# Kernel optimization log

Hardware: AMD Instinct MI355X
Metric: run time of the kernel (lower is better)

The kernel has to match this reference:

```python
import jax, jax.numpy as jnp
import numpy as np

N = 50000      # nodes
E = 800000     # edges (before self-loops)
F_IN = 256     # num_features
H = 8          # heads (conv1)
C = 32         # hidden_size per head (conv1)
OUT = 2        # conv2 out channels (1 head)
NEG_SLOPE = 0.2


def setup_inputs() -> dict:
    key = jax.random.key(0)
    ks = jax.random.split(key, 12)
    x = jax.random.normal(ks[0], (N, F_IN), jnp.float32)
    edge_index = jax.random.randint(ks[1], (2, E), 0, N, dtype=jnp.int64)

    def glorot(k, shape):
        fan = shape[0] if len(shape) == 2 else int(np.prod(shape))
        s = float(np.sqrt(6.0 / (fan + shape[-1])))
        return jax.random.uniform(k, shape, jnp.float32, -s, s)

    W1 = glorot(ks[2], (F_IN, H * C))
    att_src1 = glorot(ks[3], (H, C))
    att_dst1 = glorot(ks[4], (H, C))
    b1 = jnp.zeros((H * C,), jnp.float32)
    W2 = glorot(ks[5], (H * C, 1 * OUT))
    att_src2 = glorot(ks[6], (1, OUT))
    att_dst2 = glorot(ks[7], (1, OUT))
    b2 = jnp.zeros((OUT,), jnp.float32)
    return {"x": x, "edge_index": edge_index, "W1": W1, "att_src1": att_src1,
            "att_dst1": att_dst1, "b1": b1, "W2": W2, "att_src2": att_src2,
            "att_dst2": att_dst2, "b2": b2}


def gat_conv(x, src, dst, W, a_src, a_dst, b, heads, ch, n):
    # x: [n, f] -> projected [n, heads, ch]
    xp = (x @ W).reshape(n, heads, ch)
    alpha_src = jnp.einsum('nhc,hc->nh', xp, a_src)   # [n, H]
    alpha_dst = jnp.einsum('nhc,hc->nh', xp, a_dst)   # [n, H]
    e = jax.nn.leaky_relu(alpha_src[src] + alpha_dst[dst], NEG_SLOPE)  # [E', H]
    # segment softmax over edges grouped by destination node
    m = jax.ops.segment_max(e, dst, num_segments=n)                    # [n, H]
    p = jnp.exp(e - m[dst])
    denom = jax.ops.segment_sum(p, dst, num_segments=n)                # [n, H]
    alpha = p / denom[dst]                                             # [E', H]
    # weighted scatter-aggregate of source messages
    out = jax.ops.segment_sum(xp[src] * alpha[:, :, None], dst, num_segments=n)
    return out.reshape(n, heads * ch) + b


def reference(x, edge_index, W1, att_src1, att_dst1, b1, W2, att_src2, att_dst2, b2):
    n = x.shape[0]
    loops = jnp.arange(n, dtype=edge_index.dtype)  # GATConv add_self_loops=True
    src = jnp.concatenate([edge_index[0], loops])
    dst = jnp.concatenate([edge_index[1], loops])
    h = jax.nn.relu(gat_conv(x, src, dst, W1, att_src1, att_dst1, b1, H, C, n))
    # eval mode: F.dropout and attention dropout are identity
    return gat_conv(h, src, dst, W2, att_src2, att_dst2, b2, 1, OUT, n)
```

## Files before the change

kernel.cpp:

```cpp
#include <hip/hip_runtime.h>
#include <math.h>

#define N_NODES 50000
#define N_EDGES 800000
#define EP (N_EDGES + N_NODES)
#define NEG 0.2f
#define SCAN_BLOCKS 49

typedef __attribute__((ext_vector_type(8))) short bf16x8;
typedef __attribute__((ext_vector_type(4))) float f32x4;
typedef __attribute__((ext_vector_type(2))) float f32x2;

static __device__ __forceinline__ unsigned short bf16_rn(float f) {
    union { float f; unsigned int u; } v; v.f = f;
    unsigned int u = v.u;
    unsigned int r = (u + 0x7FFFu + ((u >> 16) & 1u)) >> 16;
    return (unsigned short)r;
}
static __device__ __forceinline__ float bf16_tof(unsigned short u) {
    union { unsigned int u; float f; } v; v.u = ((unsigned int)u) << 16;
    return v.f;
}
static __device__ __forceinline__ f32x2 bf2_unpack(unsigned int u) {
    union { unsigned int i; float f; } a, b;
    a.i = u << 16; b.i = u & 0xFFFF0000u;
    return (f32x2){a.f, b.f};
}


__global__ void k_hist(const int* __restrict__ ei, int* __restrict__ counts) {
    int e = blockIdx.x * 256 + threadIdx.x;
    if (e >= EP) return;
    int d = (e < N_EDGES) ? ei[N_EDGES + e] : (e - N_EDGES);
    atomicAdd(&counts[d], 1);
}

__global__ void k_scan_block(const int* __restrict__ counts, int* __restrict__ excl,
                             int* __restrict__ bsums) {
    __shared__ int wsum[4];
    int b = blockIdx.x, t = threadIdx.x;
    int lane = t & 63, w = t >> 6;
    int i0 = b * 1024 + t * 4;
    int v0 = (i0 + 0 < N_NODES) ? counts[i0 + 0] : 0;
    int v1 = (i0 + 1 < N_NODES) ? counts[i0 + 1] : 0;
    int v2 = (i0 + 2 < N_NODES) ? counts[i0 + 2] : 0;
    int v3 = (i0 + 3 < N_NODES) ? counts[i0 + 3] : 0;
    int s = v0 + v1 + v2 + v3;
    int incl = s;
    #pragma unroll
    for (int d = 1; d < 64; d <<= 1) {
        int u = __shfl_up(incl, d);
        if (lane >= d) incl += u;
    }
    if (lane == 63) wsum[w] = incl;
    __syncthreads();
    if (t == 0) {
        int run = 0;
        #pragma unroll
        for (int i = 0; i < 4; ++i) { int x = wsum[i]; wsum[i] = run; run += x; }
        bsums[b] = run;
    }
    __syncthreads();
    int base = wsum[w] + incl - s;
    if (i0 + 0 < N_NODES) excl[i0 + 0] = base;
    if (i0 + 1 < N_NODES) excl[i0 + 1] = base + v0;
    if (i0 + 2 < N_NODES) excl[i0 + 2] = base + v0 + v1;
    if (i0 + 3 < N_NODES) excl[i0 + 3] = base + v0 + v1 + v2;
}

__global__ void k_scan_add(int* __restrict__ row_ptr, const int* __restrict__ bsums) {
    __shared__ int soff;
    int b = blockIdx.x, t = threadIdx.x;
    if (t < 64) {
        int v = (t < SCAN_BLOCKS) ? bsums[t] : 0;
        int incl = v;
        #pragma unroll
        for (int d = 1; d < 64; d <<= 1) {
            int u = __shfl_up(incl, d);
            if (t >= d) incl += u;
        }
        if (t == b) soff = incl - v;
    }
    __syncthreads();
    int off = soff;
    int i0 = b * 1024 + t * 4;
    #pragma unroll
    for (int j = 0; j < 4; ++j)
        if (i0 + j < N_NODES) row_ptr[i0 + j] += off;
    if (b == 0 && t == 0) row_ptr[N_NODES] = EP;
}

__global__ void k_scatter(const int* __restrict__ ei, const int* __restrict__ row_ptr,
                          int* __restrict__ fill, int* __restrict__ colb) {
    int e = blockIdx.x * 256 + threadIdx.x;
    if (e >= EP) return;
    int s, d;
    if (e < N_EDGES) { s = ei[e]; d = ei[N_EDGES + e]; }
    else             { s = e - N_EDGES; d = s; }
    int pos = row_ptr[d] + atomicAdd(&fill[d], 1);
    colb[pos] = s;
}

__global__ void k_cvtWfrag(const float* __restrict__ W1, bf16x8* __restrict__ Wfrag) {
    int ft = blockIdx.x * 256 + threadIdx.x;
    int c = ft >> 10, rem = ft & 1023;
    int nt = rem >> 6, l = rem & 63;
    int n = (l & 15) * 16 + nt;
    int k0 = c * 32 + (l >> 4) * 8;
    bf16x8 f;
    #pragma unroll
    for (int j = 0; j < 8; ++j)
        f[j] = (short)bf16_rn(W1[(k0 + j) * 256 + n]);
    Wfrag[ft] = f;
}

#define GM_GRID 782
__global__ __launch_bounds__(128) void
k_gemm1m(const float* __restrict__ x, const bf16x8* __restrict__ Wfrag,
         unsigned short* __restrict__ xp1b,
         const float* __restrict__ asrc, const float* __restrict__ adst,
         float* __restrict__ as1, float* __restrict__ ad1) {
    __shared__ bf16x8 lds[1024];
    int t = threadIdx.x, l = t & 63, w = t >> 6;
    int rowbase = blockIdx.x * 64 + w * 32;
    int m = l & 15, kg = l >> 4;

    f32x4 acc0[16], acc1[16];
    #pragma unroll
    for (int nt = 0; nt < 16; ++nt) {
        acc0[nt] = (f32x4){0.f, 0.f, 0.f, 0.f};
        acc1[nt] = (f32x4){0.f, 0.f, 0.f, 0.f};
    }

    int r0 = rowbase + m;
    int r1 = rowbase + 16 + m;
    if (r0 > N_NODES - 1) r0 = N_NODES - 1;
    if (r1 > N_NODES - 1) r1 = N_NODES - 1;
    const float4* x4 = (const float4*)x;

    for (int c = 0; c < 8; ++c) {
        __syncthreads();
        const bf16x8* src = Wfrag + c * 1024;
        #pragma unroll
        for (int q = 0; q < 8; ++q)
            lds[q * 128 + t] = src[q * 128 + t];
        __syncthreads();

        int kb = (c * 32 + kg * 8) >> 2;
        float4 xa0 = x4[r0 * 64 + kb], xb0 = x4[r0 * 64 + kb + 1];
        float4 xa1 = x4[r1 * 64 + kb], xb1 = x4[r1 * 64 + kb + 1];
        bf16x8 aF0, aF1;
        aF0[0] = (short)bf16_rn(xa0.x); aF0[1] = (short)bf16_rn(xa0.y);
        aF0[2] = (short)bf16_rn(xa0.z); aF0[3] = (short)bf16_rn(xa0.w);
        aF0[4] = (short)bf16_rn(xb0.x); aF0[5] = (short)bf16_rn(xb0.y);
        aF0[6] = (short)bf16_rn(xb0.z); aF0[7] = (short)bf16_rn(xb0.w);
        aF1[0] = (short)bf16_rn(xa1.x); aF1[1] = (short)bf16_rn(xa1.y);
        aF1[2] = (short)bf16_rn(xa1.z); aF1[3] = (short)bf16_rn(xa1.w);
        aF1[4] = (short)bf16_rn(xb1.x); aF1[5] = (short)bf16_rn(xb1.y);
        aF1[6] = (short)bf16_rn(xb1.z); aF1[7] = (short)bf16_rn(xb1.w);

        #pragma unroll
        for (int nt = 0; nt < 16; ++nt) {
            bf16x8 bF = lds[nt * 64 + l];
            acc0[nt] = __builtin_amdgcn_mfma_f32_16x16x32_bf16(aF0, bF, acc0[nt], 0, 0, 0);
            acc1[nt] = __builtin_amdgcn_mfma_f32_16x16x32_bf16(aF1, bF, acc1[nt], 0, 0, 0);
        }
    }

    int cbase = l & 15, rq = l >> 4;
    float asV[16], adV[16];
    #pragma unroll
    for (int q = 0; q < 4; ++q) {
        float4 sa = ((const float4*)asrc)[cbase * 4 + q];
        float4 da = ((const float4*)adst)[cbase * 4 + q];
        asV[q * 4 + 0] = sa.x; asV[q * 4 + 1] = sa.y; asV[q * 4 + 2] = sa.z; asV[q * 4 + 3] = sa.w;
        adV[q * 4 + 0] = da.x; adV[q * 4 + 1] = da.y; adV[q * 4 + 2] = da.z; adV[q * 4 + 3] = da.w;
    }
    #pragma unroll
    for (int g = 0; g < 2; ++g) {
        f32x4* A = g ? acc1 : acc0;
        #pragma unroll
        for (int reg = 0; reg < 4; ++reg) {
            int gr = rowbase + g * 16 + rq * 4 + reg;
            unsigned int ob[8];
            float ps = 0.f, pd = 0.f;
            #pragma unroll
            for (int q = 0; q < 8; ++q) {
                float v0 = A[2 * q][reg], v1 = A[2 * q + 1][reg];
                ob[q] = (unsigned int)bf16_rn(v0) | ((unsigned int)bf16_rn(v1) << 16);
                ps = fmaf(v0, asV[2 * q], ps);     ps = fmaf(v1, asV[2 * q + 1], ps);
                pd = fmaf(v0, adV[2 * q], pd);     pd = fmaf(v1, adV[2 * q + 1], pd);
            }
            ps += __shfl_xor(ps, 1);
            pd += __shfl_xor(pd, 1);
            if (gr < N_NODES) {
                uint4* dst = (uint4*)(xp1b + gr * 256 + cbase * 16);
                dst[0] = make_uint4(ob[0], ob[1], ob[2], ob[3]);
                dst[1] = make_uint4(ob[4], ob[5], ob[6], ob[7]);
                if ((l & 1) == 0) {
                    as1[gr * 8 + (cbase >> 1)] = ps;
                    ad1[gr * 8 + (cbase >> 1)] = pd;
                }
            }
        }
    }
}

__global__ void k_agg1(const ushort4* __restrict__ xpb, const float* __restrict__ as1,
                       const float* __restrict__ ad1, const int* __restrict__ row_ptr,
                       const int* __restrict__ colb, const float* __restrict__ b1,
                       const float* __restrict__ W2, const float* __restrict__ as2w,
                       const float* __restrict__ ad2w,
                       float* __restrict__ xp2, float* __restrict__ as2,
                       float* __restrict__ ad2) {
    int t = threadIdx.x, l = t & 63, w = t >> 6;
    int n = blockIdx.x * 4 + w;
    int hidx = l >> 3;
    float adn = ad1[n * 8 + hidx];
    int start = row_ptr[n], end = row_ptr[n + 1];
    const uint2* xp2v = (const uint2*)xpb;
    f32x2 accA = {0.f, 0.f}, accB = {0.f, 0.f};
    float den = 0.f;
    int j = start;
    for (; j + 4 <= end; j += 4) {
        int s0 = colb[j], s1 = colb[j + 1], s2 = colb[j + 2], s3 = colb[j + 3];
        uint2 r0 = xp2v[s0 * 64 + l];
        uint2 r1 = xp2v[s1 * 64 + l];
        uint2 r2 = xp2v[s2 * 64 + l];
        uint2 r3 = xp2v[s3 * 64 + l];
        float e0 = as1[s0 * 8 + hidx] + adn;
        float e1 = as1[s1 * 8 + hidx] + adn;
        float e2 = as1[s2 * 8 + hidx] + adn;
        float e3 = as1[s3 * 8 + hidx] + adn;
        e0 = (e0 > 0.f) ? e0 : NEG * e0;
        e1 = (e1 > 0.f) ? e1 : NEG * e1;
        e2 = (e2 > 0.f) ? e2 : NEG * e2;
        e3 = (e3 > 0.f) ? e3 : NEG * e3;
        float p0 = __expf(e0), p1 = __expf(e1), p2 = __expf(e2), p3 = __expf(e3);
        den += (p0 + p1) + (p2 + p3);
        f32x2 q0 = {p0, p0}, q1 = {p1, p1}, q2 = {p2, p2}, q3 = {p3, p3};
        accA += q0 * bf2_unpack(r0.x);  accB += q0 * bf2_unpack(r0.y);
        accA += q1 * bf2_unpack(r1.x);  accB += q1 * bf2_unpack(r1.y);
        accA += q2 * bf2_unpack(r2.x);  accB += q2 * bf2_unpack(r2.y);
        accA += q3 * bf2_unpack(r3.x);  accB += q3 * bf2_unpack(r3.y);
    }
    for (; j < end; ++j) {
        int s = colb[j];
        uint2 r = xp2v[s * 64 + l];
        float e = as1[s * 8 + hidx] + adn;
        e = (e > 0.f) ? e : NEG * e;
        float p = __expf(e);
        den += p;
        f32x2 q = {p, p};
        accA += q * bf2_unpack(r.x);
        accB += q * bf2_unpack(r.y);
    }
    float4 bv = ((const float4*)b1)[l];
    float inv = 1.f / den;
    float4 o;
    o.x = fmaxf(accA[0] * inv + bv.x, 0.f);
    o.y = fmaxf(accA[1] * inv + bv.y, 0.f);
    o.z = fmaxf(accB[0] * inv + bv.z, 0.f);
    o.w = fmaxf(accB[1] * inv + bv.w, 0.f);
    float4 wa = ((const float4*)W2)[2 * l];
    float4 wb = ((const float4*)W2)[2 * l + 1];
    float d0 = o.x * wa.x + o.y * wa.z + o.z * wb.x + o.w * wb.z;
    float d1 = o.x * wa.y + o.y * wa.w + o.z * wb.y + o.w * wb.w;
    #pragma unroll
    for (int m = 1; m < 64; m <<= 1) {
        d0 += __shfl_xor(d0, m);
        d1 += __shfl_xor(d1, m);
    }
    if (l == 0) {
        xp2[2 * n] = d0;
        xp2[2 * n + 1] = d1;
        as2[n] = d0 * as2w[0] + d1 * as2w[1];
        ad2[n] = d0 * ad2w[0] + d1 * ad2w[1];
    }
}

__global__ void k_agg2(const float* __restrict__ xp2, const float* __restrict__ as2,
                       const float* __restrict__ ad2, const int* __restrict__ row_ptr,
                       const int* __restrict__ colb, const float* __restrict__ b2,
                       float* __restrict__ out) {
    int t = threadIdx.x, l = t & 63, w = t >> 6;
    int n = blockIdx.x * 4 + w;
    int start = row_ptr[n], end = row_ptr[n + 1];
    float adn = ad2[n];
    float a0 = 0.f, a1 = 0.f, den = 0.f;
    for (int j = start + l; j < end; j += 64) {
        int s = colb[j];
        float e = as2[s] + adn;
        e = (e > 0.f) ? e : NEG * e;
        float p = __expf(e);
        den += p;
        a0 = fmaf(p, xp2[2 * s], a0);
        a1 = fmaf(p, xp2[2 * s + 1], a1);
    }
    #pragma unroll
    for (int m = 1; m < 64; m <<= 1) {
        a0 += __shfl_xor(a0, m);
        a1 += __shfl_xor(a1, m);
        den += __shfl_xor(den, m);
    }
    if (l == 0) {
        out[2 * n] = a0 / den + b2[0];
        out[2 * n + 1] = a1 / den + b2[1];
    }
}

extern "C" void kernel_launch(void* const* d_in, const int* in_sizes, int n_in,
                              void* d_out, int out_size, void* d_ws, size_t ws_size,
                              hipStream_t stream) {
    const float* x     = (const float*)d_in[0];
    const int*   ei    = (const int*)d_in[1];
    const float* W1    = (const float*)d_in[2];
    const float* asrc1 = (const float*)d_in[3];
    const float* adst1 = (const float*)d_in[4];
    const float* b1    = (const float*)d_in[5];
    const float* W2    = (const float*)d_in[6];
    const float* asrc2 = (const float*)d_in[7];
    const float* adst2 = (const float*)d_in[8];
    const float* b2    = (const float*)d_in[9];
    float* out = (float*)d_out;

    char* ws = (char*)d_ws;
    unsigned short* xp1b = (unsigned short*)(ws + 0);
    bf16x8* Wfrag  = (bf16x8*)(ws + 25600000);
    float* as1     = (float*)(ws + 102400000);
    float* ad1     = (float*)(ws + 104000000);
    float* xp2     = (float*)(ws + 105600000);
    float* as2     = (float*)(ws + 106000000);
    float* ad2     = (float*)(ws + 106200000);
    int*   counts  = (int*)  (ws + 106400000);
    int*   fill    = (int*)  (ws + 106600000);
    int*   row_ptr = (int*)  (ws + 106800000);
    int*   colb    = (int*)  (ws + 107000064);
    int*   bsums   = (int*)  (ws + 110400064);

    hipMemsetAsync(counts, 0, 400000, stream);

    int egrid = (EP + 255) / 256;
    k_hist      <<<egrid,       256, 0, stream>>>(ei, counts);
    k_scan_block<<<SCAN_BLOCKS, 256, 0, stream>>>(counts, row_ptr, bsums);
    k_scan_add  <<<SCAN_BLOCKS, 256, 0, stream>>>(row_ptr, bsums);
    k_scatter   <<<egrid,       256, 0, stream>>>(ei, row_ptr, fill, colb);

    k_cvtWfrag  <<<32,     256, 0, stream>>>(W1, Wfrag);
    k_gemm1m    <<<GM_GRID, 128, 0, stream>>>(x, Wfrag, xp1b, asrc1, adst1, as1, ad1);
    k_agg1      <<<12500,  256, 0, stream>>>((const ushort4*)xp1b, as1, ad1, row_ptr, colb,
                                             b1, W2, asrc2, adst2, xp2, as2, ad2);
    k_agg2      <<<12500,  256, 0, stream>>>(xp2, as2, ad2, row_ptr, colb, b2, out);
}
```

Measured before the change: 290.6 us.

## Split layer-1 aggregation by head with head-major features and 16-bit column indices

The GEMM now writes projected features and attention logits in head-major order, so each head's table is a compact contiguous array. The layer-1 aggregation assigns one head per block, using the low bits of the block index so consecutive blocks take different heads. Each wave processes 8 edges in parallel with 8 lanes per edge, and per-head W2 partial products are combined with float atomics into xp2. CSR column indices shrink to 16-bit, and layer-2 uses one thread per node that recomputes the logits from xp2. The aim is a smaller per-head gather working set that stays in cache, with less index traffic. The cost is extra atomics, nondeterministic summation order, and a node count limited to 65535.

```diff
diff --git a/kernel.cpp b/kernel.cpp
--- a/kernel.cpp
+++ b/kernel.cpp
@@ -16,10 +16,6 @@
     unsigned int u = v.u;
     unsigned int r = (u + 0x7FFFu + ((u >> 16) & 1u)) >> 16;
     return (unsigned short)r;
-}
-static __device__ __forceinline__ float bf16_tof(unsigned short u) {
-    union { unsigned int u; float f; } v; v.u = ((unsigned int)u) << 16;
-    return v.f;
 }
 static __device__ __forceinline__ f32x2 bf2_unpack(unsigned int u) {
     union { unsigned int i; float f; } a, b;
@@ -91,14 +87,14 @@
 }
 
 __global__ void k_scatter(const int* __restrict__ ei, const int* __restrict__ row_ptr,
-                          int* __restrict__ fill, int* __restrict__ colb) {
+                          int* __restrict__ fill, unsigned short* __restrict__ colb) {
     int e = blockIdx.x * 256 + threadIdx.x;
     if (e >= EP) return;
     int s, d;
     if (e < N_EDGES) { s = ei[e]; d = ei[N_EDGES + e]; }
     else             { s = e - N_EDGES; d = s; }
     int pos = row_ptr[d] + atomicAdd(&fill[d], 1);
-    colb[pos] = s;
+    colb[pos] = (unsigned short)s;
 }
 
 __global__ void k_cvtWfrag(const float* __restrict__ W1, bf16x8* __restrict__ Wfrag) {
@@ -117,9 +113,9 @@
 #define GM_GRID 782
 __global__ __launch_bounds__(128) void
 k_gemm1m(const float* __restrict__ x, const bf16x8* __restrict__ Wfrag,
-         unsigned short* __restrict__ xp1b,
+         unsigned short* __restrict__ xph,
          const float* __restrict__ asrc, const float* __restrict__ adst,
-         float* __restrict__ as1, float* __restrict__ ad1) {
+         float* __restrict__ as1h, float* __restrict__ ad1h) {
     __shared__ bf16x8 lds[1024];
     int t = threadIdx.x, l = t & 63, w = t >> 6;
     int rowbase = blockIdx.x * 64 + w * 32;
@@ -168,6 +164,7 @@
     }
 
     int cbase = l & 15, rq = l >> 4;
+    int h = cbase >> 1, half = cbase & 1;
     float asV[16], adV[16];
     #pragma unroll
     for (int q = 0; q < 4; ++q) {
@@ -194,119 +191,110 @@
             ps += __shfl_xor(ps, 1);
             pd += __shfl_xor(pd, 1);
             if (gr < N_NODES) {
-                uint4* dst = (uint4*)(xp1b + gr * 256 + cbase * 16);
-                dst[0] = make_uint4(ob[0], ob[1], ob[2], ob[3]);
-                dst[1] = make_uint4(ob[4], ob[5], ob[6], ob[7]);
-                if ((l & 1) == 0) {
-                    as1[gr * 8 + (cbase >> 1)] = ps;
-                    ad1[gr * 8 + (cbase >> 1)] = pd;
+                unsigned short* row = xph + ((size_t)(h * N_NODES + gr)) * 32 + half * 16;
+                ((uint4*)row)[0] = make_uint4(ob[0], ob[1], ob[2], ob[3]);
+                ((uint4*)row)[1] = make_uint4(ob[4], ob[5], ob[6], ob[7]);
+                if (half == 0) {
+                    as1h[h * N_NODES + gr] = ps;
+                    ad1h[h * N_NODES + gr] = pd;
                 }
             }
         }
     }
 }
 
-__global__ void k_agg1(const ushort4* __restrict__ xpb, const float* __restrict__ as1,
-                       const float* __restrict__ ad1, const int* __restrict__ row_ptr,
-                       const int* __restrict__ colb, const float* __restrict__ b1,
-                       const float* __restrict__ W2, const float* __restrict__ as2w,
-                       const float* __restrict__ ad2w,
-                       float* __restrict__ xp2, float* __restrict__ as2,
-                       float* __restrict__ ad2) {
+#define AG_GRID 12504
+__global__ void k_agg1h(const unsigned short* __restrict__ xph,
+                        const float* __restrict__ as1h, const float* __restrict__ ad1h,
+                        const int* __restrict__ row_ptr, const unsigned short* __restrict__ colb,
+                        const float* __restrict__ b1, const float* __restrict__ W2,
+                        float* __restrict__ xp2) {
+    int b = blockIdx.x;
+    int h = b & 7;
     int t = threadIdx.x, l = t & 63, w = t >> 6;
-    int n = blockIdx.x * 4 + w;
-    int hidx = l >> 3;
-    float adn = ad1[n * 8 + hidx];
+    int nbase = (b >> 3) * 32 + w * 8;
+    int eg = l >> 3, q = l & 7;
+    const float* asH = as1h + h * N_NODES;
+    const float* adH = ad1h + h * N_NODES;
+    const uint2* xtab = (const uint2*)xph + (size_t)h * N_NODES * 8;
+    float4 bv = ((const float4*)b1)[h * 8 + q];
+    float4 wa = ((const float4*)W2)[h * 16 + q * 2];
+    float4 wb = ((const float4*)W2)[h * 16 + q * 2 + 1];
+
+    for (int i = 0; i < 8; ++i) {
+        int n = nbase + i;
+        if (n >= N_NODES) break;
+        float adn = adH[n];
+        int start = row_ptr[n], end = row_ptr[n + 1];
+        f32x2 aA = {0.f, 0.f}, aB = {0.f, 0.f};
+        float den = 0.f;
+        for (int j = start; j < end; j += 8) {
+            int je = j + eg;
+            if (je < end) {
+                int s = colb[je];
+                float e = asH[s] + adn;
+                e = (e > 0.f) ? e : NEG * e;
+                float p = __expf(e);
+                den += p;
+                uint2 r = xtab[s * 8 + q];
+                f32x2 pp = {p, p};
+                aA += pp * bf2_unpack(r.x);
+                aB += pp * bf2_unpack(r.y);
+            }
+        }
+        #pragma unroll
+        for (int m = 8; m < 64; m <<= 1) {
+            aA[0] += __shfl_xor(aA[0], m);
+            aA[1] += __shfl_xor(aA[1], m);
+            aB[0] += __shfl_xor(aB[0], m);
+            aB[1] += __shfl_xor(aB[1], m);
+            den   += __shfl_xor(den, m);
+        }
+        float inv = 1.f / den;
+        float o0 = fmaxf(aA[0] * inv + bv.x, 0.f);
+        float o1 = fmaxf(aA[1] * inv + bv.y, 0.f);
+        float o2 = fmaxf(aB[0] * inv + bv.z, 0.f);
+        float o3 = fmaxf(aB[1] * inv + bv.w, 0.f);
+        float d0 = o0 * wa.x + o1 * wa.z + o2 * wb.x + o3 * wb.z;
+        float d1 = o0 * wa.y + o1 * wa.w + o2 * wb.y + o3 * wb.w;
+        #pragma unroll
+        for (int m = 1; m < 8; m <<= 1) {
+            d0 += __shfl_xor(d0, m);
+            d1 += __shfl_xor(d1, m);
+        }
+        if (l == 0) {
+            atomicAdd(&xp2[2 * n], d0);
+            atomicAdd(&xp2[2 * n + 1], d1);
+        }
+    }
+}
+
+__global__ void k_agg2(const float* __restrict__ xp2, const int* __restrict__ row_ptr,
+                       const unsigned short* __restrict__ colb,
+                       const float* __restrict__ as2w, const float* __restrict__ ad2w,
+                       const float* __restrict__ b2, float* __restrict__ out) {
+    int n = blockIdx.x * 256 + threadIdx.x;
+    if (n >= N_NODES) return;
+    float w_s0 = as2w[0], w_s1 = as2w[1];
+    float w_d0 = ad2w[0], w_d1 = ad2w[1];
+    const float2* xpv = (const float2*)xp2;
+    float2 me = xpv[n];
+    float adn = me.x * w_d0 + me.y * w_d1;
     int start = row_ptr[n], end = row_ptr[n + 1];
-    const uint2* xp2v = (const uint2*)xpb;
-    f32x2 accA = {0.f, 0.f}, accB = {0.f, 0.f};
-    float den = 0.f;
-    int j = start;
-    for (; j + 4 <= end; j += 4) {
-        int s0 = colb[j], s1 = colb[j + 1], s2 = colb[j + 2], s3 = colb[j + 3];
-        uint2 r0 = xp2v[s0 * 64 + l];
-        uint2 r1 = xp2v[s1 * 64 + l];
-        uint2 r2 = xp2v[s2 * 64 + l];
-        uint2 r3 = xp2v[s3 * 64 + l];
-        float e0 = as1[s0 * 8 + hidx] + adn;
-        float e1 = as1[s1 * 8 + hidx] + adn;
-        float e2 = as1[s2 * 8 + hidx] + adn;
-        float e3 = as1[s3 * 8 + hidx] + adn;
-        e0 = (e0 > 0.f) ? e0 : NEG * e0;
-        e1 = (e1 > 0.f) ? e1 : NEG * e1;
-        e2 = (e2 > 0.f) ? e2 : NEG * e2;
-        e3 = (e3 > 0.f) ? e3 : NEG * e3;
-        float p0 = __expf(e0), p1 = __expf(e1), p2 = __expf(e2), p3 = __expf(e3);
-        den += (p0 + p1) + (p2 + p3);
-        f32x2 q0 = {p0, p0}, q1 = {p1, p1}, q2 = {p2, p2}, q3 = {p3, p3};
-        accA += q0 * bf2_unpack(r0.x);  accB += q0 * bf2_unpack(r0.y);
-        accA += q1 * bf2_unpack(r1.x);  accB += q1 * bf2_unpack(r1.y);
-        accA += q2 * bf2_unpack(r2.x);  accB += q2 * bf2_unpack(r2.y);
-        accA += q3 * bf2_unpack(r3.x);  accB += q3 * bf2_unpack(r3.y);
-    }
-    for (; j < end; ++j) {
+    float b20 = b2[0], b21 = b2[1];
+    float a0 = 0.f, a1 = 0.f, den = 0.f;
+    for (int j = start; j < end; ++j) {
         int s = colb[j];
-        uint2 r = xp2v[s * 64 + l];
-        float e = as1[s * 8 + hidx] + adn;
+        float2 v = xpv[s];
+        float e = v.x * w_s0 + v.y * w_s1 + adn;
         e = (e > 0.f) ? e : NEG * e;
         float p = __expf(e);
         den += p;
-        f32x2 q = {p, p};
-        accA += q * bf2_unpack(r.x);
-        accB += q * bf2_unpack(r.y);
-    }
-    float4 bv = ((const float4*)b1)[l];
+        a0 = fmaf(p, v.x, a0);
+        a1 = fmaf(p, v.y, a1);
+    }
     float inv = 1.f / den;
-    float4 o;
-    o.x = fmaxf(accA[0] * inv + bv.x, 0.f);
-    o.y = fmaxf(accA[1] * inv + bv.y, 0.f);
-    o.z = fmaxf(accB[0] * inv + bv.z, 0.f);
-    o.w = fmaxf(accB[1] * inv + bv.w, 0.f);
-    float4 wa = ((const float4*)W2)[2 * l];
-    float4 wb = ((const float4*)W2)[2 * l + 1];
-    float d0 = o.x * wa.x + o.y * wa.z + o.z * wb.x + o.w * wb.z;
-    float d1 = o.x * wa.y + o.y * wa.w + o.z * wb.y + o.w * wb.w;
-    #pragma unroll
-    for (int m = 1; m < 64; m <<= 1) {
-        d0 += __shfl_xor(d0, m);
-        d1 += __shfl_xor(d1, m);
-    }
-    if (l == 0) {
-        xp2[2 * n] = d0;
-        xp2[2 * n + 1] = d1;
-        as2[n] = d0 * as2w[0] + d1 * as2w[1];
-        ad2[n] = d0 * ad2w[0] + d1 * ad2w[1];
-    }
-}
-
-__global__ void k_agg2(const float* __restrict__ xp2, const float* __restrict__ as2,
-                       const float* __restrict__ ad2, const int* __restrict__ row_ptr,
-                       const int* __restrict__ colb, const float* __restrict__ b2,
-                       float* __restrict__ out) {
-    int t = threadIdx.x, l = t & 63, w = t >> 6;
-    int n = blockIdx.x * 4 + w;
-    int start = row_ptr[n], end = row_ptr[n + 1];
-    float adn = ad2[n];
-    float a0 = 0.f, a1 = 0.f, den = 0.f;
-    for (int j = start + l; j < end; j += 64) {
-        int s = colb[j];
-        float e = as2[s] + adn;
-        e = (e > 0.f) ? e : NEG * e;
-        float p = __expf(e);
-        den += p;
-        a0 = fmaf(p, xp2[2 * s], a0);
-        a1 = fmaf(p, xp2[2 * s + 1], a1);
-    }
-    #pragma unroll
-    for (int m = 1; m < 64; m <<= 1) {
-        a0 += __shfl_xor(a0, m);
-        a1 += __shfl_xor(a1, m);
-        den += __shfl_xor(den, m);
-    }
-    if (l == 0) {
-        out[2 * n] = a0 / den + b2[0];
-        out[2 * n + 1] = a1 / den + b2[1];
-    }
+    ((float2*)out)[n] = make_float2(a0 * inv + b20, a1 * inv + b21);
 }
 
 extern "C" void kernel_launch(void* const* d_in, const int* in_sizes, int n_in,
@@ -325,30 +313,28 @@
     float* out = (float*)d_out;
 
     char* ws = (char*)d_ws;
-    unsigned short* xp1b = (unsigned short*)(ws + 0);
+    unsigned short* xph  = (unsigned short*)(ws + 0);
     bf16x8* Wfrag  = (bf16x8*)(ws + 25600000);
-    float* as1     = (float*)(ws + 102400000);
-    float* ad1     = (float*)(ws + 104000000);
-    float* xp2     = (float*)(ws + 105600000);
-    float* as2     = (float*)(ws + 106000000);
-    float* ad2     = (float*)(ws + 106200000);
-    int*   counts  = (int*)  (ws + 106400000);
-    int*   fill    = (int*)  (ws + 106600000);
-    int*   row_ptr = (int*)  (ws + 106800000);
-    int*   colb    = (int*)  (ws + 107000064);
-    int*   bsums   = (int*)  (ws + 110400064);
+    float* as1h    = (float*)(ws + 25800000);
+    float* ad1h    = (float*)(ws + 27400000);
+    float* xp2     = (float*)(ws + 29000000);
+    int*   counts  = (int*)  (ws + 29400000);
+    int*   fill    = (int*)  (ws + 29600000);
+    int*   row_ptr = (int*)  (ws + 29800000);
+    unsigned short* colb = (unsigned short*)(ws + 30000064);
+    int*   bsums   = (int*)  (ws + 31700064);
 
     hipMemsetAsync(counts, 0, 400000, stream);
+    hipMemsetAsync(xp2, 0, 400000, stream);
 
     int egrid = (EP + 255) / 256;
     k_hist      <<<egrid,       256, 0, stream>>>(ei, counts);
     k_scan_block<<<SCAN_BLOCKS, 256, 0, stream>>>(counts, row_ptr, bsums);
     k_scan_add  <<<SCAN_BLOCKS, 256, 0, stream>>>(row_ptr, bsums);
     k_scatter   <<<egrid,       256, 0, stream>>>(ei, row_ptr, fill, colb);
-
     k_cvtWfrag  <<<32,     256, 0, stream>>>(W1, Wfrag);
-    k_gemm1m    <<<GM_GRID, 128, 0, stream>>>(x, Wfrag, xp1b, asrc1, adst1, as1, ad1);
-    k_agg1      <<<12500,  256, 0, stream>>>((const ushort4*)xp1b, as1, ad1, row_ptr, colb,
-                                             b1, W2, asrc2, adst2, xp2, as2, ad2);
-    k_agg2      <<<12500,  256, 0, stream>>>(xp2, as2, ad2, row_ptr, colb, b2, out);
-}
+
+    k_gemm1m <<<GM_GRID, 128, 0, stream>>>(x, Wfrag, xph, asrc1, adst1, as1h, ad1h);
+    k_agg1h  <<<AG_GRID, 256, 0, stream>>>(xph, as1h, ad1h, row_ptr, colb, b1, W2, xp2);
+    k_agg2   <<<196,     256, 0, stream>>>(xp2, row_ptr, colb, asrc2, adst2, b2, out);
+}
```

Measured after the change: 377.5 us. 29.9% more time.
